# Optimization experiments

Hardware: AMD Instinct MI355X
Metric: run time of the kernel (lower is better)

## Reference

```python
import jax, jax.numpy as jnp
import numpy as np

B, S, HID = 2, 2048, 2048
H, HK, D = 16, 4, 128  # num_heads, num_kv_heads, head_dim
G = H // HK            # GQA group size


def _make_rope(B, S, D):
    pos = jnp.arange(S, dtype=jnp.float32)
    inv_freq = 1.0 / (10000.0 ** (jnp.arange(0, D, 2, dtype=jnp.float32) / D))
    freqs = pos[:, None] * inv_freq[None, :]          # [S, D/2]
    emb = jnp.concatenate([freqs, freqs], axis=-1)     # [S, D]
    cos = jnp.broadcast_to(jnp.cos(emb)[None], (B, S, D))
    sin = jnp.broadcast_to(jnp.sin(emb)[None], (B, S, D))
    return cos, sin


def setup_inputs() -> dict:
    key = jax.random.key(0)
    k0, k1, k2 = jax.random.split(key, 3)
    hidden_states = jax.random.normal(k0, (B, S, HID), dtype=jnp.float32)
    cos, sin = _make_rope(B, S, D)
    w_qkv = jax.random.normal(k1, ((H + 2 * HK) * D, HID), dtype=jnp.float32) * 0.02
    b_qkv = jnp.zeros(((H + 2 * HK) * D,), dtype=jnp.float32)
    w_o = jax.random.normal(k2, (HID, HID), dtype=jnp.float32) * 0.02
    b_o = jnp.zeros((HID,), dtype=jnp.float32)
    return {"hidden_states": hidden_states, "cos": cos, "sin": sin,
            "w_qkv": w_qkv, "b_qkv": b_qkv, "w_o": w_o, "b_o": b_o}


def _rotate_half(x):
    x1, x2 = jnp.split(x, 2, axis=-1)
    return jnp.concatenate([-x2, x1], axis=-1)


def reference(hidden_states, cos, sin, w_qkv, b_qkv, w_o, b_o):
    b, s, _ = hidden_states.shape
    qkv = jnp.einsum('bsh,oh->bso', hidden_states, w_qkv) + b_qkv
    q, k, v = jnp.split(qkv, [H * D, (H + HK) * D], axis=-1)
    # [B, heads, S, D]
    q = q.reshape(b, s, H, D).transpose(0, 2, 1, 3)
    k = k.reshape(b, s, HK, D).transpose(0, 2, 1, 3)
    v = v.reshape(b, s, HK, D).transpose(0, 2, 1, 3)
    # RoPE (cos/sin broadcast over head axis)
    c = cos[:, None, :, :]
    sn = sin[:, None, :, :]
    q = q * c + _rotate_half(q) * sn
    k = k * c + _rotate_half(k) * sn
    # GQA attention without materializing repeated K/V: group q heads
    qg = q.reshape(b, HK, G, s, D)
    scale = 1.0 / jnp.sqrt(jnp.float32(D))
    scores = jnp.einsum('bkgqd,bkpd->bkgqp', qg, k) * scale  # [B,HK,G,S,S]
    probs = jax.nn.softmax(scores, axis=-1)
    out = jnp.einsum('bkgqp,bkpd->bkgqd', probs, v)           # [B,HK,G,S,D]
    out = out.reshape(b, H, s, D).transpose(0, 2, 1, 3).reshape(b, s, H * D)
    return jnp.einsum('bsh,oh->bso', out, w_o) + b_o
```

## Files before the change

kernel.cpp:

```cpp
#include <hip/hip_runtime.h>
#include <hip/hip_bf16.h>
#include <stdint.h>

typedef __bf16 bf16x8 __attribute__((ext_vector_type(8)));
typedef float f32x4 __attribute__((ext_vector_type(4)));
typedef float f32x16 __attribute__((ext_vector_type(16)));
typedef float f32x4v __attribute__((ext_vector_type(4)));
typedef unsigned short u16;
typedef unsigned int u32;
typedef u16 u16x8 __attribute__((ext_vector_type(8)));
typedef u32 u32x4 __attribute__((ext_vector_type(4)));

#define B_ 2
#define S_ 2048
#define HID_ 2048
#define H_ 16
#define HK_ 4
#define D_ 128
#define NQKV_ 3072

__device__ __forceinline__ u16 f2bf(float f) {
  u32 u = __builtin_bit_cast(u32, f);
  u32 r = (u + 0x7fffu + ((u >> 16) & 1u)) >> 16;
  return (u16)r;
}
__device__ __forceinline__ float bf2f(u16 v) {
  u32 u = ((u32)v) << 16;
  return __builtin_bit_cast(float, u);
}
__device__ __forceinline__ u32 cvtpk(float lo, float hi) {
  u32 r;
  asm("v_cvt_pk_bf16_f32 %0, %1, %2" : "=v"(r) : "v"(lo), "v"(hi));
  return r;
}
__device__ __forceinline__ void gload_lds16(const void* g, void* l) {
  __builtin_amdgcn_global_load_lds((const __attribute__((address_space(1))) void*)g,
                                   (__attribute__((address_space(3))) void*)l, 16, 0, 0);
}

__global__ __launch_bounds__(256) void k_cvt3(const float* __restrict__ a, u16* __restrict__ oa, int na,
                                              const float* __restrict__ b, u16* __restrict__ ob, int nb,
                                              const float* __restrict__ c, u16* __restrict__ oc, int nc) {
  int total = na + nb + nc;
  for (int i = blockIdx.x * 256 + threadIdx.x; i < total; i += gridDim.x * 256) {
    const float* src;
    u16* dst;
    int j = i;
    if (j < na) { src = a; dst = oa; }
    else if (j < na + nb) { j -= na; src = b; dst = ob; }
    else { j -= na + nb; src = c; dst = oc; }
    const f32x4v* p = (const f32x4v*)(src + (size_t)j * 8);
    f32x4v x = p[0], y = p[1];
    u16x8 w;
    w[0] = f2bf(x[0]); w[1] = f2bf(x[1]); w[2] = f2bf(x[2]); w[3] = f2bf(x[3]);
    w[4] = f2bf(y[0]); w[5] = f2bf(y[1]); w[6] = f2bf(y[2]); w[7] = f2bf(y[3]);
    *(u16x8*)(dst + (size_t)j * 8) = w;
  }
}

template <int ISSUES>
__device__ __forceinline__ void stage_half(const u16* __restrict__ src, int K, char* ldsb, int tid) {
#pragma unroll
  for (int i = 0; i < ISSUES; ++i) {
    int off = i * 8192 + tid * 16;
    int r = off >> 7, cb = off & 127;
    int scb = cb ^ ((r & 7) << 4);
    gload_lds16((const char*)(src + (size_t)r * K) + scb, ldsb + i * 8192 + (tid & ~63) * 16);
  }
}

template <int BM, typename CT>
__global__ __launch_bounds__(512, 1) void k_gemm8p(const u16* __restrict__ A, const u16* __restrict__ Bm,
                                                   const float* __restrict__ bias, CT* __restrict__ C,
                                                   int M, int N, int K) {
  constexpr int HAR = BM / 2;
  constexpr int AHB = HAR * 128;
  constexpr int AISS = AHB / 8192;
  constexpr int MREP = BM / 32;
  constexpr int MQ = MREP / 4;
  constexpr int DB = 2 * AHB + 32768;
  __shared__ __attribute__((aligned(16))) char lds[2 * DB];
  const int tid = threadIdx.x, lane = tid & 63;
  const int wid = tid >> 6, wm = wid >> 2, wn = wid & 3;
  const int l15 = lane & 15, l4 = lane >> 4;
  const int row0 = blockIdx.y * BM, col0 = blockIdx.x * 256;
  const int NT = K >> 6;

  f32x4 acc[MREP][4] = {};

  auto stageA = [&](int t, int h) {
    stage_half<AISS>(A + (size_t)(row0 + h * HAR) * K + t * 64, K, lds + (t & 1) * DB + h * AHB, tid);
  };
  auto stageB = [&](int t, int h) {
    stage_half<2>(Bm + (size_t)(col0 + h * 128) * K + t * 64, K, lds + (t & 1) * DB + 2 * AHB + h * 16384, tid);
  };

  stageA(0, 0); stageA(0, 1); stageB(0, 0); stageB(0, 1);
  if (NT > 1) { stageB(1, 0); stageB(1, 1); }
  if (NT > 1) asm volatile("s_waitcnt vmcnt(4)" ::: "memory");
  else        asm volatile("s_waitcnt vmcnt(0)" ::: "memory");
  __builtin_amdgcn_s_barrier();

  const char* myA = lds + wm * AHB;
  const char* myB = lds + 2 * AHB + (wn >> 1) * 16384;
  const int rBb = (wn & 1) * 64;

  for (int t = 0; t < NT; ++t) {
    const int d = t & 1;
    const char* Ab = myA + d * DB;
    const char* Bb = myB + d * DB;
    bf16x8 bfr[4][2];
#pragma unroll
    for (int j = 0; j < 4; ++j) {
      if (j == 0) {
#pragma unroll
        for (int n = 0; n < 4; ++n)
#pragma unroll
          for (int ks = 0; ks < 2; ++ks) {
            int r = rBb + n * 16 + l15;
            bfr[n][ks] = *(const bf16x8*)(Bb + r * 128 + ((ks * 64 + l4 * 16) ^ ((r & 7) << 4)));
          }
      }
      bf16x8 afr[MQ][2];
#pragma unroll
      for (int mq = 0; mq < MQ; ++mq)
#pragma unroll
        for (int ks = 0; ks < 2; ++ks) {
          int r = (j * MQ + mq) * 16 + l15;
          afr[mq][ks] = *(const bf16x8*)(Ab + r * 128 + ((ks * 64 + l4 * 16) ^ ((r & 7) << 4)));
        }
      if (j == 0) { if (t + 1 < NT) stageA(t + 1, 0); }
      else if (j == 1) { if (t + 1 < NT) stageA(t + 1, 1); }
      else if (j == 2) { if (t + 2 < NT) stageB(t + 2, 0); }
      else {
        if (t + 2 < NT) { stageB(t + 2, 1); asm volatile("s_waitcnt vmcnt(4)" ::: "memory"); }
        else             asm volatile("s_waitcnt vmcnt(0)" ::: "memory");
      }
      __builtin_amdgcn_s_barrier();
      asm volatile("s_waitcnt lgkmcnt(0)" ::: "memory");
      __builtin_amdgcn_s_setprio(1);
#pragma unroll
      for (int mq = 0; mq < MQ; ++mq)
#pragma unroll
        for (int ks = 0; ks < 2; ++ks)
#pragma unroll
          for (int n = 0; n < 4; ++n)
            acc[j * MQ + mq][n] =
                __builtin_amdgcn_mfma_f32_16x16x32_bf16(afr[mq][ks], bfr[n][ks], acc[j * MQ + mq][n], 0, 0, 0);
      __builtin_amdgcn_s_setprio(0);
      __builtin_amdgcn_s_barrier();
    }
  }

#pragma unroll
  for (int m = 0; m < MREP; ++m) {
    int grow = row0 + wm * HAR + m * 16 + l4 * 4;
#pragma unroll
    for (int n = 0; n < 4; ++n) {
      int gcol = col0 + wn * 64 + n * 16 + l15;
      float bv = bias[gcol];
#pragma unroll
      for (int r2 = 0; r2 < 4; ++r2) {
        float v = acc[m][n][r2] + bv;
        if constexpr (sizeof(CT) == 2) C[(size_t)(grow + r2) * N + gcol] = (CT)f2bf(v);
        else                           C[(size_t)(grow + r2) * N + gcol] = v;
      }
    }
  }
}

__global__ __launch_bounds__(256) void k_rope_split(const u16* __restrict__ qkv,
                                                    const float* __restrict__ cosb,
                                                    const float* __restrict__ sinb,
                                                    u16* __restrict__ Qb, u16* __restrict__ Kb,
                                                    u16* __restrict__ Vt) {
  const int bs = blockIdx.x;
  const int b = bs >> 11, s = bs & 2047;
  const size_t base = (size_t)bs * NQKV_;
  const size_t cs = (size_t)bs * D_;
  const float qscale = 0.08838834764831845f;
  for (int p = threadIdx.x; p < H_ * 64; p += 256) {
    int h = p >> 6, d = p & 63;
    float f1 = bf2f(qkv[base + h * D_ + d]);
    float f2 = bf2f(qkv[base + h * D_ + 64 + d]);
    float c1 = cosb[cs + d], s1 = sinb[cs + d];
    float c2 = cosb[cs + 64 + d], s2 = sinb[cs + 64 + d];
    size_t o = ((size_t)(b * H_ + h) * S_ + s) * D_ + d;
    Qb[o] = f2bf((f1 * c1 - f2 * s1) * qscale);
    Qb[o + 64] = f2bf((f2 * c2 + f1 * s2) * qscale);
  }
  for (int p = threadIdx.x; p < HK_ * 64; p += 256) {
    int hk = p >> 6, d = p & 63;
    float f1 = bf2f(qkv[base + H_ * D_ + hk * D_ + d]);
    float f2 = bf2f(qkv[base + H_ * D_ + hk * D_ + 64 + d]);
    float c1 = cosb[cs + d], s1 = sinb[cs + d];
    float c2 = cosb[cs + 64 + d], s2 = sinb[cs + 64 + d];
    size_t o = ((size_t)(b * HK_ + hk) * S_ + s) * D_ + d;
    Kb[o] = f2bf(f1 * c1 - f2 * s1);
    Kb[o + 64] = f2bf(f2 * c2 + f1 * s2);
  }
  for (int p = threadIdx.x; p < HK_ * D_; p += 256) {
    int hk = p >> 7, d = p & 127;
    Vt[((size_t)(b * HK_ + hk) * D_ + d) * S_ + s] = qkv[base + H_ * D_ + HK_ * D_ + hk * D_ + d];
  }
}

__global__ __launch_bounds__(512, 2) void k_attn(const u16* __restrict__ Qb, const u16* __restrict__ Kb,
                                                 const u16* __restrict__ Vt, u16* __restrict__ Ob) {
  __shared__ __attribute__((aligned(16))) char lds[65536];
  const int qt = blockIdx.x;
  const int bh = blockIdx.y;
  const int b = bh >> 4, h = bh & 15, hk = h >> 2;
  const int tid = threadIdx.x, lane = tid & 63, wid = tid >> 6;
  const int l31 = lane & 31, hi = lane >> 5;

  const int qrow = qt * 256 + wid * 32 + l31;
  const u16* qptr = Qb + ((size_t)(b * H_ + h) * S_ + qrow) * D_;
  bf16x8 qf[8];
#pragma unroll
  for (int ks = 0; ks < 8; ++ks) qf[ks] = *(const bf16x8*)(qptr + ks * 16 + hi * 8);

  const u16* kbase = Kb + (size_t)(b * HK_ + hk) * S_ * D_;
  const u16* vbase = Vt + (size_t)(b * HK_ + hk) * D_ * S_;

  int krow[2], kc[2], vrow[2], vc[2];
#pragma unroll
  for (int i = 0; i < 2; ++i) {
    int s = tid + i * 512;
    krow[i] = s >> 4; kc[i] = s & 15;
    vrow[i] = s >> 3; vc[i] = s & 7;
  }

  f32x16 o[4] = {};
  float mrun = -1e30f, lrun = 0.f;

  bf16x8 kreg[2], vreg[2];
#pragma unroll
  for (int i = 0; i < 2; ++i) {
    kreg[i] = *(const bf16x8*)(kbase + (size_t)krow[i] * D_ + kc[i] * 8);
    vreg[i] = *(const bf16x8*)(vbase + (size_t)vrow[i] * S_ + vc[i] * 8);
  }
#pragma unroll
  for (int i = 0; i < 2; ++i) {
    *(bf16x8*)(lds + ((krow[i] * 256 + kc[i] * 16) ^ ((krow[i] & 15) << 4))) = kreg[i];
    *(bf16x8*)(lds + 16384 + ((vrow[i] * 128 + vc[i] * 16) ^ ((vrow[i] & 7) << 4))) = vreg[i];
  }
  __syncthreads();

  for (int kt = 0; kt < 32; ++kt) {
    const int cur = kt & 1;
    const char* lKc = lds + cur * 32768;
    const char* lVc = lKc + 16384;

    if (kt < 31) {
#pragma unroll
      for (int i = 0; i < 2; ++i) {
        kreg[i] = *(const bf16x8*)(kbase + (size_t)((kt + 1) * 64 + krow[i]) * D_ + kc[i] * 8);
        vreg[i] = *(const bf16x8*)(vbase + (size_t)vrow[i] * S_ + (kt + 1) * 64 + vc[i] * 8);
      }
    }

    f32x16 sc[2] = {};
    __builtin_amdgcn_s_setprio(1);
#pragma unroll
    for (int ks = 0; ks < 8; ++ks) {
#pragma unroll
      for (int T = 0; T < 2; ++T) {
        int row = T * 32 + l31;
        bf16x8 kf = *(const bf16x8*)(lKc + ((row * 256 + ks * 32 + hi * 16) ^ ((row & 15) << 4)));
        sc[T] = __builtin_amdgcn_mfma_f32_32x32x16_bf16(kf, qf[ks], sc[T], 0, 0, 0);
      }
    }
    __builtin_amdgcn_s_setprio(0);

    float pmax = sc[0][0];
#pragma unroll
    for (int r = 1; r < 16; ++r) pmax = fmaxf(pmax, sc[0][r]);
#pragma unroll
    for (int r = 0; r < 16; ++r) pmax = fmaxf(pmax, sc[1][r]);
    pmax = fmaxf(pmax, __shfl_xor(pmax, 32));
    if (__any(pmax > mrun + 8.f)) {
      float mn = fmaxf(mrun, pmax);
      float alpha = __expf(mrun - mn);
      mrun = mn;
      lrun *= alpha;
#pragma unroll
      for (int dt = 0; dt < 4; ++dt)
#pragma unroll
        for (int r = 0; r < 16; ++r) o[dt][r] *= alpha;
    }
    float rs = 0.f;
#pragma unroll
    for (int T = 0; T < 2; ++T)
#pragma unroll
      for (int r = 0; r < 16; ++r) {
        float p = __expf(sc[T][r] - mrun);
        sc[T][r] = p;
        rs += p;
      }
    rs += __shfl_xor(rs, 32);
    lrun += rs;

    bf16x8 pf[4];
#pragma unroll
    for (int T = 0; T < 2; ++T) {
#pragma unroll
      for (int g = 0; g < 2; ++g) {
        u32 a0 = cvtpk(sc[T][8 * g + 0], sc[T][8 * g + 1]);
        u32 a1 = cvtpk(sc[T][8 * g + 2], sc[T][8 * g + 3]);
        u32 a2 = cvtpk(sc[T][8 * g + 4], sc[T][8 * g + 5]);
        u32 a3 = cvtpk(sc[T][8 * g + 6], sc[T][8 * g + 7]);
        u32 x0 = (u32)__shfl_xor((int)a0, 32);
        u32 x1 = (u32)__shfl_xor((int)a1, 32);
        u32 x2 = (u32)__shfl_xor((int)a2, 32);
        u32 x3 = (u32)__shfl_xor((int)a3, 32);
        u32 s0 = hi ? x2 : a0;
        u32 s1 = hi ? x3 : a1;
        u32 s2 = hi ? a2 : x0;
        u32 s3 = hi ? a3 : x1;
        u32x4 w = {s0, s1, s2, s3};
        pf[T * 2 + g] = __builtin_bit_cast(bf16x8, w);
      }
    }

    __builtin_amdgcn_s_setprio(1);
#pragma unroll
    for (int ks2 = 0; ks2 < 4; ++ks2) {
#pragma unroll
      for (int dt = 0; dt < 4; ++dt) {
        int row = dt * 32 + l31;
        bf16x8 vf = *(const bf16x8*)(lVc + ((row * 128 + ks2 * 32 + hi * 16) ^ ((row & 7) << 4)));
        o[dt] = __builtin_amdgcn_mfma_f32_32x32x16_bf16(vf, pf[ks2], o[dt], 0, 0, 0);
      }
    }
    __builtin_amdgcn_s_setprio(0);

    if (kt < 31) {
      char* nK = lds + (cur ^ 1) * 32768;
      char* nV = nK + 16384;
#pragma unroll
      for (int i = 0; i < 2; ++i) {
        *(bf16x8*)(nK + ((krow[i] * 256 + kc[i] * 16) ^ ((krow[i] & 15) << 4))) = kreg[i];
        *(bf16x8*)(nV + ((vrow[i] * 128 + vc[i] * 16) ^ ((vrow[i] & 7) << 4))) = vreg[i];
      }
    }
    __syncthreads();
  }

  float inv = 1.0f / lrun;
  char* myreg = lds + wid * 8192;
#pragma unroll
  for (int dt = 0; dt < 4; ++dt)
#pragma unroll
    for (int t = 0; t < 8; ++t) {
      u32 w = cvtpk(o[dt][2 * t] * inv, o[dt][2 * t + 1] * inv);
      int d0 = dt * 32 + 2 * (t & 1) + 8 * (t >> 1) + 4 * hi;
      *(u32*)(myreg + ((l31 * 256 + d0 * 2) ^ ((l31 & 15) << 4))) = w;
    }
  asm volatile("s_waitcnt lgkmcnt(0)");
  {
    int q = lane >> 1, hf = lane & 1;
    int srow = qt * 256 + wid * 32 + q;
    u16* orow = Ob + ((size_t)(b * S_ + srow)) * HID_ + h * 128 + hf * 64;
#pragma unroll
    for (int i = 0; i < 8; ++i) {
      bf16x8 vv = *(const bf16x8*)(myreg + ((q * 256 + hf * 128 + i * 16) ^ ((q & 15) << 4)));
      *(bf16x8*)(orow + i * 8) = vv;
    }
  }
}

extern "C" void kernel_launch(void* const* d_in, const int* in_sizes, int n_in,
                              void* d_out, int out_size, void* d_ws, size_t ws_size,
                              hipStream_t stream) {
  const float* hs = (const float*)d_in[0];
  const float* cosb = (const float*)d_in[1];
  const float* sinb = (const float*)d_in[2];
  const float* w_qkv = (const float*)d_in[3];
  const float* b_qkv = (const float*)d_in[4];
  const float* w_o = (const float*)d_in[5];
  const float* b_o = (const float*)d_in[6];
  float* out = (float*)d_out;

  char* ws = (char*)d_ws;
  u16* Xb    = (u16*)ws;
  u16* Wqkvb = (u16*)(ws + 16777216);
  u16* Wob   = (u16*)(ws + 29360128);
  u16* qkvb  = (u16*)(ws + 37748736);
  u16* Qb    = (u16*)(ws + 62914560);
  u16* Kb    = (u16*)(ws + 79691776);
  u16* Vt    = (u16*)(ws + 83886080);
  u16* Ob = Xb;

  hipLaunchKernelGGL(k_cvt3, dim3(2048), dim3(256), 0, stream,
                     hs, Xb, (B_ * S_ * HID_) / 8,
                     w_qkv, Wqkvb, (NQKV_ * HID_) / 8,
                     w_o, Wob, (HID_ * HID_) / 8);
  hipLaunchKernelGGL((k_gemm8p<256, u16>), dim3(NQKV_ / 256, (B_ * S_) / 256), dim3(512), 0, stream,
                     Xb, Wqkvb, b_qkv, qkvb, B_ * S_, NQKV_, HID_);
  hipLaunchKernelGGL(k_rope_split, dim3(B_ * S_), dim3(256), 0, stream, qkvb, cosb, sinb, Qb, Kb, Vt);
  hipLaunchKernelGGL(k_attn, dim3(S_ / 256, B_ * H_), dim3(512), 0, stream, Qb, Kb, Vt, Ob);
  hipLaunchKernelGGL((k_gemm8p<128, float>), dim3(HID_ / 256, (B_ * S_) / 128), dim3(512), 0, stream,
                     Ob, Wob, b_o, out, B_ * S_, HID_, HID_);
}
```

Measured before the change: 219.7 us.

## Software-pipeline attention loop to overlap QK of next tile with softmax/PV

Restructures the flash-attention inner loop so the QK^T MFMAs for tile t are issued alongside the softmax and PV of tile t-1. Two ping-ponged score accumulator sets carry scores across iterations, and the global-to-LDS staging is rescheduled with a prologue and epilogue. The aim is to hide exp and shuffle latency behind matrix-core work. In exchange it adds a second barrier per iteration and raises register pressure from the extra live accumulators, which could lower occupancy or cause spills.

```diff
diff --git a/kernel.cpp b/kernel.cpp
--- a/kernel.cpp
+++ b/kernel.cpp
@@ -235,49 +235,42 @@
   float mrun = -1e30f, lrun = 0.f;
 
   bf16x8 kreg[2], vreg[2];
-#pragma unroll
-  for (int i = 0; i < 2; ++i) {
-    kreg[i] = *(const bf16x8*)(kbase + (size_t)krow[i] * D_ + kc[i] * 8);
-    vreg[i] = *(const bf16x8*)(vbase + (size_t)vrow[i] * S_ + vc[i] * 8);
-  }
-#pragma unroll
-  for (int i = 0; i < 2; ++i) {
-    *(bf16x8*)(lds + ((krow[i] * 256 + kc[i] * 16) ^ ((krow[i] & 15) << 4))) = kreg[i];
-    *(bf16x8*)(lds + 16384 + ((vrow[i] * 128 + vc[i] * 16) ^ ((vrow[i] & 7) << 4))) = vreg[i];
-  }
-  __syncthreads();
-
-  for (int kt = 0; kt < 32; ++kt) {
-    const int cur = kt & 1;
-    const char* lKc = lds + cur * 32768;
-    const char* lVc = lKc + 16384;
-
-    if (kt < 31) {
-#pragma unroll
-      for (int i = 0; i < 2; ++i) {
-        kreg[i] = *(const bf16x8*)(kbase + (size_t)((kt + 1) * 64 + krow[i]) * D_ + kc[i] * 8);
-        vreg[i] = *(const bf16x8*)(vbase + (size_t)vrow[i] * S_ + (kt + 1) * 64 + vc[i] * 8);
-      }
-    }
-
-    f32x16 sc[2] = {};
-    __builtin_amdgcn_s_setprio(1);
+
+  auto stage_load = [&](int t) {
+#pragma unroll
+    for (int i = 0; i < 2; ++i) {
+      kreg[i] = *(const bf16x8*)(kbase + (size_t)(t * 64 + krow[i]) * D_ + kc[i] * 8);
+      vreg[i] = *(const bf16x8*)(vbase + (size_t)vrow[i] * S_ + t * 64 + vc[i] * 8);
+    }
+  };
+  auto stage_write = [&](int t) {
+    char* nK = lds + (t & 1) * 32768;
+    char* nV = nK + 16384;
+#pragma unroll
+    for (int i = 0; i < 2; ++i) {
+      *(bf16x8*)(nK + ((krow[i] * 256 + kc[i] * 16) ^ ((krow[i] & 15) << 4))) = kreg[i];
+      *(bf16x8*)(nV + ((vrow[i] * 128 + vc[i] * 16) ^ ((vrow[i] & 7) << 4))) = vreg[i];
+    }
+  };
+  auto qk = [&](const char* lK, f32x16& c0, f32x16& c1) {
+    f32x16 zz = {};
+    c0 = zz; c1 = zz;
 #pragma unroll
     for (int ks = 0; ks < 8; ++ks) {
-#pragma unroll
-      for (int T = 0; T < 2; ++T) {
-        int row = T * 32 + l31;
-        bf16x8 kf = *(const bf16x8*)(lKc + ((row * 256 + ks * 32 + hi * 16) ^ ((row & 15) << 4)));
-        sc[T] = __builtin_amdgcn_mfma_f32_32x32x16_bf16(kf, qf[ks], sc[T], 0, 0, 0);
-      }
-    }
-    __builtin_amdgcn_s_setprio(0);
-
-    float pmax = sc[0][0];
-#pragma unroll
-    for (int r = 1; r < 16; ++r) pmax = fmaxf(pmax, sc[0][r]);
-#pragma unroll
-    for (int r = 0; r < 16; ++r) pmax = fmaxf(pmax, sc[1][r]);
+      int rowa = l31;
+      bf16x8 kf0 = *(const bf16x8*)(lK + ((rowa * 256 + ks * 32 + hi * 16) ^ ((rowa & 15) << 4)));
+      c0 = __builtin_amdgcn_mfma_f32_32x32x16_bf16(kf0, qf[ks], c0, 0, 0, 0);
+      int rowb = 32 + l31;
+      bf16x8 kf1 = *(const bf16x8*)(lK + ((rowb * 256 + ks * 32 + hi * 16) ^ ((rowb & 15) << 4)));
+      c1 = __builtin_amdgcn_mfma_f32_32x32x16_bf16(kf1, qf[ks], c1, 0, 0, 0);
+    }
+  };
+  auto finish = [&](f32x16& p0, f32x16& p1, const char* lV) {
+    float pmax = p0[0];
+#pragma unroll
+    for (int r = 1; r < 16; ++r) pmax = fmaxf(pmax, p0[r]);
+#pragma unroll
+    for (int r = 0; r < 16; ++r) pmax = fmaxf(pmax, p1[r]);
     pmax = fmaxf(pmax, __shfl_xor(pmax, 32));
     if (__any(pmax > mrun + 8.f)) {
       float mn = fmaxf(mrun, pmax);
@@ -291,61 +284,87 @@
     }
     float rs = 0.f;
 #pragma unroll
-    for (int T = 0; T < 2; ++T)
-#pragma unroll
-      for (int r = 0; r < 16; ++r) {
-        float p = __expf(sc[T][r] - mrun);
-        sc[T][r] = p;
-        rs += p;
-      }
+    for (int r = 0; r < 16; ++r) { float p = __expf(p0[r] - mrun); p0[r] = p; rs += p; }
+#pragma unroll
+    for (int r = 0; r < 16; ++r) { float p = __expf(p1[r] - mrun); p1[r] = p; rs += p; }
     rs += __shfl_xor(rs, 32);
     lrun += rs;
 
     bf16x8 pf[4];
 #pragma unroll
-    for (int T = 0; T < 2; ++T) {
-#pragma unroll
-      for (int g = 0; g < 2; ++g) {
-        u32 a0 = cvtpk(sc[T][8 * g + 0], sc[T][8 * g + 1]);
-        u32 a1 = cvtpk(sc[T][8 * g + 2], sc[T][8 * g + 3]);
-        u32 a2 = cvtpk(sc[T][8 * g + 4], sc[T][8 * g + 5]);
-        u32 a3 = cvtpk(sc[T][8 * g + 6], sc[T][8 * g + 7]);
-        u32 x0 = (u32)__shfl_xor((int)a0, 32);
-        u32 x1 = (u32)__shfl_xor((int)a1, 32);
-        u32 x2 = (u32)__shfl_xor((int)a2, 32);
-        u32 x3 = (u32)__shfl_xor((int)a3, 32);
-        u32 s0 = hi ? x2 : a0;
-        u32 s1 = hi ? x3 : a1;
-        u32 s2 = hi ? a2 : x0;
-        u32 s3 = hi ? a3 : x1;
-        u32x4 w = {s0, s1, s2, s3};
-        pf[T * 2 + g] = __builtin_bit_cast(bf16x8, w);
-      }
+    for (int g = 0; g < 2; ++g) {
+      u32 a0 = cvtpk(p0[8 * g + 0], p0[8 * g + 1]);
+      u32 a1 = cvtpk(p0[8 * g + 2], p0[8 * g + 3]);
+      u32 a2 = cvtpk(p0[8 * g + 4], p0[8 * g + 5]);
+      u32 a3 = cvtpk(p0[8 * g + 6], p0[8 * g + 7]);
+      u32 x0 = (u32)__shfl_xor((int)a0, 32);
+      u32 x1 = (u32)__shfl_xor((int)a1, 32);
+      u32 x2 = (u32)__shfl_xor((int)a2, 32);
+      u32 x3 = (u32)__shfl_xor((int)a3, 32);
+      u32 s0 = hi ? x2 : a0;
+      u32 s1 = hi ? x3 : a1;
+      u32 s2 = hi ? a2 : x0;
+      u32 s3 = hi ? a3 : x1;
+      u32x4 w = {s0, s1, s2, s3};
+      pf[g] = __builtin_bit_cast(bf16x8, w);
+    }
+#pragma unroll
+    for (int g = 0; g < 2; ++g) {
+      u32 a0 = cvtpk(p1[8 * g + 0], p1[8 * g + 1]);
+      u32 a1 = cvtpk(p1[8 * g + 2], p1[8 * g + 3]);
+      u32 a2 = cvtpk(p1[8 * g + 4], p1[8 * g + 5]);
+      u32 a3 = cvtpk(p1[8 * g + 6], p1[8 * g + 7]);
+      u32 x0 = (u32)__shfl_xor((int)a0, 32);
+      u32 x1 = (u32)__shfl_xor((int)a1, 32);
+      u32 x2 = (u32)__shfl_xor((int)a2, 32);
+      u32 x3 = (u32)__shfl_xor((int)a3, 32);
+      u32 s0 = hi ? x2 : a0;
+      u32 s1 = hi ? x3 : a1;
+      u32 s2 = hi ? a2 : x0;
+      u32 s3 = hi ? a3 : x1;
+      u32x4 w = {s0, s1, s2, s3};
+      pf[2 + g] = __builtin_bit_cast(bf16x8, w);
     }
 
     __builtin_amdgcn_s_setprio(1);
 #pragma unroll
-    for (int ks2 = 0; ks2 < 4; ++ks2) {
+    for (int ks2 = 0; ks2 < 4; ++ks2)
 #pragma unroll
       for (int dt = 0; dt < 4; ++dt) {
         int row = dt * 32 + l31;
-        bf16x8 vf = *(const bf16x8*)(lVc + ((row * 128 + ks2 * 32 + hi * 16) ^ ((row & 7) << 4)));
+        bf16x8 vf = *(const bf16x8*)(lV + ((row * 128 + ks2 * 32 + hi * 16) ^ ((row & 7) << 4)));
         o[dt] = __builtin_amdgcn_mfma_f32_32x32x16_bf16(vf, pf[ks2], o[dt], 0, 0, 0);
       }
-    }
     __builtin_amdgcn_s_setprio(0);
-
-    if (kt < 31) {
-      char* nK = lds + (cur ^ 1) * 32768;
-      char* nV = nK + 16384;
-#pragma unroll
-      for (int i = 0; i < 2; ++i) {
-        *(bf16x8*)(nK + ((krow[i] * 256 + kc[i] * 16) ^ ((krow[i] & 15) << 4))) = kreg[i];
-        *(bf16x8*)(nV + ((vrow[i] * 128 + vc[i] * 16) ^ ((vrow[i] & 7) << 4))) = vreg[i];
-      }
-    }
+  };
+
+  f32x16 scA0, scA1, scB0, scB1;
+  stage_load(0);
+  stage_write(0);
+  stage_load(1);
+  __syncthreads();
+  qk(lds, scA0, scA1);
+  stage_write(1);
+  stage_load(2);
+  __syncthreads();
+
+  auto iter = [&](int t, f32x16& c0, f32x16& c1, f32x16& p0, f32x16& p1) {
+    qk(lds + (t & 1) * 32768, c0, c1);
+    finish(p0, p1, lds + ((t & 1) ^ 1) * 32768 + 16384);
     __syncthreads();
-  }
+    if (t < 31) stage_write(t + 1);
+    if (t < 30) stage_load(t + 2);
+    __syncthreads();
+  };
+
+  iter(1, scB0, scB1, scA0, scA1);
+#pragma unroll 1
+  for (int i = 0; i < 15; ++i) {
+    iter(2 + 2 * i, scA0, scA1, scB0, scB1);
+    iter(3 + 2 * i, scB0, scB1, scA0, scA1);
+  }
+  finish(scB0, scB1, lds + 32768 + 16384);
+  __syncthreads();
 
   float inv = 1.0f / lrun;
   char* myreg = lds + wid * 8192;
```

After: 219.5 us. Within noise of the previous version (-0.1%).

## Swizzle GEMM workgroup order and vectorize RoPE split kernel loads/stores

Applied to the files above, without the earlier changes.

The GEMM kernel remaps block IDs so that consecutive workgroups are spread across XCDs in contiguous tile chunks, aiming at better L2 locality on the multi-die MI355X. The RoPE/split kernel now has each thread handle 8 contiguous bf16 elements with 16-byte vector loads and stores for Q and K, replacing scalar strided loops. V transposition still uses scalar strided stores. The swizzle assumes the block count divides evenly by 8.

```diff
diff --git a/kernel.cpp b/kernel.cpp
--- a/kernel.cpp
+++ b/kernel.cpp
@@ -83,7 +83,11 @@
   const int tid = threadIdx.x, lane = tid & 63;
   const int wid = tid >> 6, wm = wid >> 2, wn = wid & 3;
   const int l15 = lane & 15, l4 = lane >> 4;
-  const int row0 = blockIdx.y * BM, col0 = blockIdx.x * 256;
+  const int nwg = gridDim.x * gridDim.y;
+  const int bid = blockIdx.y * gridDim.x + blockIdx.x;
+  const int wgid = (bid & 7) * (nwg >> 3) + (bid >> 3);
+  const int bx = wgid % gridDim.x, by = wgid / gridDim.x;
+  const int row0 = by * BM, col0 = bx * 256;
   const int NT = K >> 6;
 
   f32x4 acc[MREP][4] = {};
@@ -178,30 +182,42 @@
   const int b = bs >> 11, s = bs & 2047;
   const size_t base = (size_t)bs * NQKV_;
   const size_t cs = (size_t)bs * D_;
+  const int tid = threadIdx.x;
   const float qscale = 0.08838834764831845f;
-  for (int p = threadIdx.x; p < H_ * 64; p += 256) {
-    int h = p >> 6, d = p & 63;
-    float f1 = bf2f(qkv[base + h * D_ + d]);
-    float f2 = bf2f(qkv[base + h * D_ + 64 + d]);
-    float c1 = cosb[cs + d], s1 = sinb[cs + d];
-    float c2 = cosb[cs + 64 + d], s2 = sinb[cs + 64 + d];
-    size_t o = ((size_t)(b * H_ + h) * S_ + s) * D_ + d;
-    Qb[o] = f2bf((f1 * c1 - f2 * s1) * qscale);
-    Qb[o + 64] = f2bf((f2 * c2 + f1 * s2) * qscale);
-  }
-  for (int p = threadIdx.x; p < HK_ * 64; p += 256) {
-    int hk = p >> 6, d = p & 63;
-    float f1 = bf2f(qkv[base + H_ * D_ + hk * D_ + d]);
-    float f2 = bf2f(qkv[base + H_ * D_ + hk * D_ + 64 + d]);
-    float c1 = cosb[cs + d], s1 = sinb[cs + d];
-    float c2 = cosb[cs + 64 + d], s2 = sinb[cs + 64 + d];
-    size_t o = ((size_t)(b * HK_ + hk) * S_ + s) * D_ + d;
-    Kb[o] = f2bf(f1 * c1 - f2 * s1);
-    Kb[o + 64] = f2bf(f2 * c2 + f1 * s2);
-  }
-  for (int p = threadIdx.x; p < HK_ * D_; p += 256) {
-    int hk = p >> 7, d = p & 127;
-    Vt[((size_t)(b * HK_ + hk) * D_ + d) * S_ + s] = qkv[base + H_ * D_ + HK_ * D_ + hk * D_ + d];
+
+  if (tid < 160) {
+    const bool isq = tid < 128;
+    const int idx = isq ? tid : (tid - 128);
+    const int hh = idx >> 3, d0 = (idx & 7) * 8;
+    const size_t srcb = base + (isq ? 0 : H_ * D_) + hh * D_;
+    bf16x8 x1 = *(const bf16x8*)(qkv + srcb + d0);
+    bf16x8 x2 = *(const bf16x8*)(qkv + srcb + d0 + 64);
+    u16x8 y1, y2;
+    const u16x8 u1 = __builtin_bit_cast(u16x8, x1);
+    const u16x8 u2 = __builtin_bit_cast(u16x8, x2);
+    const float sc = isq ? qscale : 1.0f;
+#pragma unroll
+    for (int i = 0; i < 8; ++i) {
+      float f1 = bf2f(u1[i]), f2 = bf2f(u2[i]);
+      float c1 = cosb[cs + d0 + i], s1 = sinb[cs + d0 + i];
+      float c2 = cosb[cs + 64 + d0 + i], s2 = sinb[cs + 64 + d0 + i];
+      y1[i] = f2bf((f1 * c1 - f2 * s1) * sc);
+      y2[i] = f2bf((f2 * c2 + f1 * s2) * sc);
+    }
+    size_t o;
+    if (isq) o = ((size_t)(b * H_ + hh) * S_ + s) * D_ + d0;
+    else     o = ((size_t)(b * HK_ + hh) * S_ + s) * D_ + d0;
+    u16* dst = isq ? Qb : Kb;
+    *(u16x8*)(dst + o) = y1;
+    *(u16x8*)(dst + o + 64) = y2;
+  } else if (tid < 224) {
+    const int idx = tid - 160;
+    const int hk = idx >> 4, d0 = (idx & 15) * 8;
+    bf16x8 xv = *(const bf16x8*)(qkv + base + (H_ + HK_) * D_ + hk * D_ + d0);
+    const u16x8 uv = __builtin_bit_cast(u16x8, xv);
+    u16* vb = Vt + (size_t)(b * HK_ + hk) * D_ * S_ + s;
+#pragma unroll
+    for (int i = 0; i < 8; ++i) vb[(size_t)(d0 + i) * S_] = uv[i];
   }
 }
 
```

Result: no change. 217.6 us, median of 2 (-0.9%).
